# Kernel optimization log

Hardware: AMD Instinct MI355X
Metric: run time of the kernel (lower is better)

## Reference

```python
import jax, jax.numpy as jnp
import numpy as np

B, T, D, H = 2048, 200, 64, 64


def setup_inputs() -> dict:
    key = jax.random.key(0)
    ks = jax.random.split(key, 5)
    rnn_input = jax.random.normal(ks[0], (B, T, D), dtype=jnp.float32)
    sequence_length = jax.random.randint(ks[1], (B,), 0, T, dtype=jnp.int32)
    att_score = jax.random.uniform(ks[2], (B, T, 1), dtype=jnp.float32)
    # glorot-uniform-style init for kernels; TF VecAttGRUCell uses constant 1.0 gate bias
    s = np.float32(np.sqrt(6.0 / (D + H + 2 * H)))
    gate_kernel = jax.random.uniform(ks[3], (D + H, 2 * H), jnp.float32, -s, s)
    gate_bias = jnp.ones((2 * H,), jnp.float32)
    sc = np.float32(np.sqrt(6.0 / (D + H + H)))
    cand_kernel = jax.random.uniform(ks[4], (D + H, H), jnp.float32, -sc, sc)
    cand_bias = jnp.zeros((H,), jnp.float32)
    return dict(rnn_input=rnn_input, sequence_length=sequence_length,
                att_score=att_score, gate_kernel=gate_kernel, gate_bias=gate_bias,
                cand_kernel=cand_kernel, cand_bias=cand_bias)


def _augru(rnn_input, sequence_length, att_score, gate_kernel, gate_bias, cand_kernel, cand_bias):
    # rnn_input: [B,T,D], att_score: [B,T,1], sequence_length: [B]
    Bn, Tn, _ = rnn_input.shape
    Hn = cand_kernel.shape[1]
    x_t = jnp.swapaxes(rnn_input, 0, 1)   # [T,B,D]
    a_t = jnp.swapaxes(att_score, 0, 1)   # [T,B,1]
    t_idx = jnp.arange(Tn)
    h0 = jnp.zeros((Bn, Hn), rnn_input.dtype)

    def step(h, inp):
        x, a, t = inp
        gates = jax.nn.sigmoid(jnp.concatenate([x, h], axis=-1) @ gate_kernel + gate_bias)
        r, u = jnp.split(gates, 2, axis=-1)                       # [B,H] each
        c = jnp.tanh(jnp.concatenate([x, r * h], axis=-1) @ cand_kernel + cand_bias)
        u_hat = (1.0 - a) * u                                      # attention-modulated update gate
        new_h = u_hat * h + (1.0 - u_hat) * c
        valid = (t < sequence_length)[:, None]                     # dynamic_rnn semantics
        h_next = jnp.where(valid, new_h, h)                        # freeze state past seq len
        out = jnp.where(valid, new_h, jnp.zeros_like(new_h))       # zero outputs past seq len
        return h_next, out

    h_last, outs = jax.lax.scan(step, h0, (x_t, a_t, t_idx))
    return jnp.swapaxes(outs, 0, 1), h_last  # [B,T,H], [B,H]


def reference(rnn_input, sequence_length, att_score, gate_kernel, gate_bias, cand_kernel, cand_bias):
    outputs, _ = _augru(rnn_input, sequence_length, att_score,
                        gate_kernel, gate_bias, cand_kernel, cand_bias)
    return outputs  # return_sequence=True
```

## Files before the change

kernel.cpp:

```cpp
#include <hip/hip_runtime.h>

#define Tn 200
#define Dn 64
#define Hn 64
#define CC 16

typedef _Float16 half2v __attribute__((ext_vector_type(2)));
typedef _Float16 half8v __attribute__((ext_vector_type(8)));
typedef float    f32x4  __attribute__((ext_vector_type(4)));

__device__ __forceinline__ float fast_sigmoid(float v) {
    return __builtin_amdgcn_rcpf(1.0f + __expf(-v));
}
__device__ __forceinline__ float fast_tanh(float v) {
    return 1.0f - 2.0f * __builtin_amdgcn_rcpf(1.0f + __expf(2.0f * v));
}
__device__ __forceinline__ void wave_lds_fence() {
    asm volatile("s_waitcnt lgkmcnt(0)" ::: "memory");
}

__device__ __forceinline__ half8v cvt8(const float4 a, const float4 b) {
    return half8v{(_Float16)a.x, (_Float16)a.y, (_Float16)a.z, (_Float16)a.w,
                  (_Float16)b.x, (_Float16)b.y, (_Float16)b.z, (_Float16)b.w};
}

__global__ __launch_bounds__(256, 4)
void augru_proj_mfma(const float* __restrict__ x,
                     const int*   __restrict__ slen,
                     const float* __restrict__ gk,
                     const float* __restrict__ gb,
                     const float* __restrict__ ck,
                     const float* __restrict__ cb,
                     _Float16*    __restrict__ P,
                     int nrows, int nchunks)
{
    const int tid  = threadIdx.x;
    const int w    = tid >> 6;
    const int lane = tid & 63;
    const int lm   = lane & 15;
    const int kq   = lane >> 4;

    half8v bf[3][2];
    float  bias[3];
#pragma unroll
    for (int nt = 0; nt < 3; ++nt) {
        const int n = w * 48 + nt * 16 + lm;
#pragma unroll
        for (int kh = 0; kh < 2; ++kh) {
            const int kb = kh * 32 + kq * 8;
            half8v f;
#pragma unroll
            for (int e = 0; e < 8; ++e) {
                const int k = kb + e;
                const float v = (n < 128) ? gk[k * 128 + n]
                                          : ck[k * 64 + (n - 128)];
                f[e] = (_Float16)v;
            }
            bf[nt][kh] = f;
        }
        bias[nt] = (n < 128) ? gb[n] : cb[n - 128];
    }

    for (int chunk = blockIdx.x; chunk < nchunks; chunk += gridDim.x) {
        const int rb0 = chunk * 64;
#pragma unroll
        for (int sub = 0; sub < 4; ++sub) {
            const int rb = rb0 + sub * 16;

            const int rowv = rb + lm;
            const int bv   = rowv / Tn;
            const int tv   = rowv - bv * Tn;
            const bool v   = (rowv < nrows) && (tv < slen[bv]);
            if (__ballot(v) == 0ull) continue;

            const int rowA = min(rb + lm, nrows - 1);
            const float* xr = x + (size_t)rowA * Dn + kq * 8;
            const float4 q0 = *(const float4*)(xr);
            const float4 q1 = *(const float4*)(xr + 4);
            const float4 q2 = *(const float4*)(xr + 32);
            const float4 q3 = *(const float4*)(xr + 36);
            const half8v a0 = cvt8(q0, q1);
            const half8v a1 = cvt8(q2, q3);

            f32x4 acc[3];
#pragma unroll
            for (int nt = 0; nt < 3; ++nt) {
                f32x4 c = {bias[nt], bias[nt], bias[nt], bias[nt]};
                c = __builtin_amdgcn_mfma_f32_16x16x32_f16(a0, bf[nt][0], c, 0, 0, 0);
                c = __builtin_amdgcn_mfma_f32_16x16x32_f16(a1, bf[nt][1], c, 0, 0, 0);
                acc[nt] = c;
            }

#pragma unroll
            for (int r = 0; r < 4; ++r) {
                const int row = rb + kq * 4 + r;
                const int bb  = row / Tn;
                const int tt  = row - bb * Tn;
                if (row < nrows && tt < slen[bb]) {
                    _Float16* Pt = P + (size_t)row * 192 + w * 48 + lm;
                    Pt[0]  = (_Float16)acc[0][r];
                    Pt[16] = (_Float16)acc[1][r];
                    Pt[32] = (_Float16)acc[2][r];
                }
            }
        }
    }
}

__global__ __launch_bounds__(64, 2)
void augru_rec(const _Float16* __restrict__ P,
               const int*     __restrict__ slen,
               const float*   __restrict__ att,
               const float*   __restrict__ gk,
               const float*   __restrict__ ck,
               float*         __restrict__ out)
{
    const int b = blockIdx.x;
    const int j = threadIdx.x;

    __shared__ __align__(16) _Float16 s_h[Hn];
    __shared__ __align__(16) _Float16 s_rh[Hn];

    half2v wr[32], wu[32], wc[32];
#pragma unroll
    for (int m = 0; m < 32; ++m) {
        const int k = 64 + 2 * m;
        wr[m] = half2v{(_Float16)gk[(k + 0) * 128 + j],
                       (_Float16)gk[(k + 1) * 128 + j]};
        wu[m] = half2v{(_Float16)gk[(k + 0) * 128 + 64 + j],
                       (_Float16)gk[(k + 1) * 128 + 64 + j]};
        wc[m] = half2v{(_Float16)ck[(k + 0) * 64 + j],
                       (_Float16)ck[(k + 1) * 64 + j]};
    }

    const int len = slen[b];
    const _Float16* Prow = P   + (size_t)b * Tn * 192;
    const float*    arow = att + (size_t)b * Tn;
    float*          orow = out + (size_t)b * Tn * Hn;

    float h = 0.0f;

    _Float16 pr_n = (_Float16)0, pu_n = (_Float16)0, pc_n = (_Float16)0;
    float a_n = 0.0f;
    if (len > 0) {
        pr_n = Prow[j]; pu_n = Prow[64 + j]; pc_n = Prow[128 + j];
        a_n  = arow[0];
    }

    for (int t = 0; t < len; ++t) {
        const float pr = (float)pr_n;
        const float pu = (float)pu_n;
        const float pc = (float)pc_n;
        const float a  = a_n;
        const int tn = min(t + 1, len - 1);
        const _Float16* Pt = Prow + tn * 192;
        pr_n = Pt[j]; pu_n = Pt[64 + j]; pc_n = Pt[128 + j];
        a_n  = arow[tn];

        s_h[j] = (_Float16)h;
        wave_lds_fence();

        float r0 = pr, r1 = 0.f, u0 = pu, u1 = 0.f;
        const half8v* hv = (const half8v*)s_h;
#pragma unroll
        for (int m8 = 0; m8 < 8; ++m8) {
            const half8v v = hv[m8];
            const half2v p0 = __builtin_shufflevector(v, v, 0, 1);
            const half2v p1 = __builtin_shufflevector(v, v, 2, 3);
            const half2v p2 = __builtin_shufflevector(v, v, 4, 5);
            const half2v p3 = __builtin_shufflevector(v, v, 6, 7);
            const int m = m8 * 4;
            r0 = __builtin_amdgcn_fdot2(p0, wr[m + 0], r0, false);
            r1 = __builtin_amdgcn_fdot2(p1, wr[m + 1], r1, false);
            r0 = __builtin_amdgcn_fdot2(p2, wr[m + 2], r0, false);
            r1 = __builtin_amdgcn_fdot2(p3, wr[m + 3], r1, false);
            u0 = __builtin_amdgcn_fdot2(p0, wu[m + 0], u0, false);
            u1 = __builtin_amdgcn_fdot2(p1, wu[m + 1], u1, false);
            u0 = __builtin_amdgcn_fdot2(p2, wu[m + 2], u0, false);
            u1 = __builtin_amdgcn_fdot2(p3, wu[m + 3], u1, false);
        }
        const float rg = fast_sigmoid(r0 + r1);
        const float ug = fast_sigmoid(u0 + u1);

        s_rh[j] = (_Float16)(rg * h);
        wave_lds_fence();

        float c0 = pc, c1 = 0.f;
        const half8v* rv = (const half8v*)s_rh;
#pragma unroll
        for (int m8 = 0; m8 < 8; ++m8) {
            const half8v v = rv[m8];
            const half2v p0 = __builtin_shufflevector(v, v, 0, 1);
            const half2v p1 = __builtin_shufflevector(v, v, 2, 3);
            const half2v p2 = __builtin_shufflevector(v, v, 4, 5);
            const half2v p3 = __builtin_shufflevector(v, v, 6, 7);
            const int m = m8 * 4;
            c0 = __builtin_amdgcn_fdot2(p0, wc[m + 0], c0, false);
            c1 = __builtin_amdgcn_fdot2(p1, wc[m + 1], c1, false);
            c0 = __builtin_amdgcn_fdot2(p2, wc[m + 2], c0, false);
            c1 = __builtin_amdgcn_fdot2(p3, wc[m + 3], c1, false);
        }
        const float cg = fast_tanh(c0 + c1);

        const float uh = (1.0f - a) * ug;
        h = uh * h + (1.0f - uh) * cg;
        orow[t * Hn + j] = h;
        wave_lds_fence();
    }

    float4 z;
    z.x = z.y = z.z = z.w = 0.0f;
    float* tail = orow + len * Hn;
    const int total = (Tn - len) * Hn;
    for (int i = j * 4; i < total; i += 64 * 4) {
        *(float4*)(tail + i) = z;
    }
}

__global__ __launch_bounds__(128, 2)
void augru_fused_fb(const float* __restrict__ x, const int* __restrict__ slen,
                    const float* __restrict__ att, const float* __restrict__ gk,
                    const float* __restrict__ gb, const float* __restrict__ ck,
                    const float* __restrict__ cb, float* __restrict__ out)
{
    const int b    = blockIdx.x;
    const int tid  = threadIdx.x;
    const int wave = tid >> 6;
    const int j    = tid & 63;

    __shared__ float s_P[2][CC][3][Hn];
    __shared__ __align__(16) _Float16 s_h[Hn];
    __shared__ __align__(16) _Float16 s_rh[Hn];

    const int len     = slen[b];
    const int nchunks = (len + CC - 1) / CC;
    const float* xrow = x   + (size_t)b * Tn * Dn;
    const float* arow = att + (size_t)b * Tn;
    float*       orow = out + (size_t)b * Tn * Hn;

    if (wave == 0) {
        half2v wr[32], wu[32], wc[32];
#pragma unroll
        for (int m = 0; m < 32; ++m) {
            const int k = 2 * m;
            wr[m] = half2v{(_Float16)gk[(k + 0) * 128 + j], (_Float16)gk[(k + 1) * 128 + j]};
            wu[m] = half2v{(_Float16)gk[(k + 0) * 128 + 64 + j], (_Float16)gk[(k + 1) * 128 + 64 + j]};
            wc[m] = half2v{(_Float16)ck[(k + 0) * 64 + j], (_Float16)ck[(k + 1) * 64 + j]};
        }
        const float br = gb[j], bu = gb[64 + j], bc = cb[j];
        for (int c = 0; c < nchunks; ++c) {
            const int t0 = c * CC, tend = min(len, t0 + CC);
            for (int t = t0; t < tend; ++t) {
                const float4* xv = (const float4*)(xrow + t * Dn);
                float r0 = br, r1 = 0.f, u0 = bu, u1 = 0.f, c0 = bc, c1 = 0.f;
#pragma unroll
                for (int kk = 0; kk < 16; ++kk) {
                    const float4 q = xv[kk];
                    const half2v p0 = half2v{(_Float16)q.x, (_Float16)q.y};
                    const half2v p1 = half2v{(_Float16)q.z, (_Float16)q.w};
                    const int m = 2 * kk;
                    r0 = __builtin_amdgcn_fdot2(p0, wr[m], r0, false);
                    r1 = __builtin_amdgcn_fdot2(p1, wr[m + 1], r1, false);
                    u0 = __builtin_amdgcn_fdot2(p0, wu[m], u0, false);
                    u1 = __builtin_amdgcn_fdot2(p1, wu[m + 1], u1, false);
                    c0 = __builtin_amdgcn_fdot2(p0, wc[m], c0, false);
                    c1 = __builtin_amdgcn_fdot2(p1, wc[m + 1], c1, false);
                }
                const int lt = t - t0;
                s_P[c & 1][lt][0][j] = r0 + r1;
                s_P[c & 1][lt][1][j] = u0 + u1;
                s_P[c & 1][lt][2][j] = c0 + c1;
            }
            __syncthreads();
        }
    } else {
        half2v wr[32], wu[32], wc[32];
#pragma unroll
        for (int m = 0; m < 32; ++m) {
            const int k = 64 + 2 * m;
            wr[m] = half2v{(_Float16)gk[(k + 0) * 128 + j], (_Float16)gk[(k + 1) * 128 + j]};
            wu[m] = half2v{(_Float16)gk[(k + 0) * 128 + 64 + j], (_Float16)gk[(k + 1) * 128 + 64 + j]};
            wc[m] = half2v{(_Float16)ck[(k + 0) * 64 + j], (_Float16)ck[(k + 1) * 64 + j]};
        }
        float h = 0.0f;
        for (int c = 0; c < nchunks; ++c) {
            __syncthreads();
            const int t0 = c * CC, tend = min(len, t0 + CC);
            for (int t = t0; t < tend; ++t) {
                const int lt = t - t0;
                const float pr = s_P[c & 1][lt][0][j];
                const float pu = s_P[c & 1][lt][1][j];
                const float pc = s_P[c & 1][lt][2][j];
                const float a  = arow[t];
                s_h[j] = (_Float16)h;
                wave_lds_fence();
                float r0 = pr, r1 = 0.f, u0 = pu, u1 = 0.f;
                const half8v* hv = (const half8v*)s_h;
#pragma unroll
                for (int m8 = 0; m8 < 8; ++m8) {
                    const half8v v = hv[m8];
                    const half2v p0 = __builtin_shufflevector(v, v, 0, 1);
                    const half2v p1 = __builtin_shufflevector(v, v, 2, 3);
                    const half2v p2 = __builtin_shufflevector(v, v, 4, 5);
                    const half2v p3 = __builtin_shufflevector(v, v, 6, 7);
                    const int m = m8 * 4;
                    r0 = __builtin_amdgcn_fdot2(p0, wr[m + 0], r0, false);
                    r1 = __builtin_amdgcn_fdot2(p1, wr[m + 1], r1, false);
                    r0 = __builtin_amdgcn_fdot2(p2, wr[m + 2], r0, false);
                    r1 = __builtin_amdgcn_fdot2(p3, wr[m + 3], r1, false);
                    u0 = __builtin_amdgcn_fdot2(p0, wu[m + 0], u0, false);
                    u1 = __builtin_amdgcn_fdot2(p1, wu[m + 1], u1, false);
                    u0 = __builtin_amdgcn_fdot2(p2, wu[m + 2], u0, false);
                    u1 = __builtin_amdgcn_fdot2(p3, wu[m + 3], u1, false);
                }
                const float rg = fast_sigmoid(r0 + r1);
                const float ug = fast_sigmoid(u0 + u1);
                s_rh[j] = (_Float16)(rg * h);
                wave_lds_fence();
                float c0 = pc, c1 = 0.f;
                const half8v* rv = (const half8v*)s_rh;
#pragma unroll
                for (int m8 = 0; m8 < 8; ++m8) {
                    const half8v v = rv[m8];
                    const half2v p0 = __builtin_shufflevector(v, v, 0, 1);
                    const half2v p1 = __builtin_shufflevector(v, v, 2, 3);
                    const half2v p2 = __builtin_shufflevector(v, v, 4, 5);
                    const half2v p3 = __builtin_shufflevector(v, v, 6, 7);
                    const int m = m8 * 4;
                    c0 = __builtin_amdgcn_fdot2(p0, wc[m + 0], c0, false);
                    c1 = __builtin_amdgcn_fdot2(p1, wc[m + 1], c1, false);
                    c0 = __builtin_amdgcn_fdot2(p2, wc[m + 2], c0, false);
                    c1 = __builtin_amdgcn_fdot2(p3, wc[m + 3], c1, false);
                }
                const float cg = fast_tanh(c0 + c1);
                const float uh = (1.0f - a) * ug;
                h = uh * h + (1.0f - uh) * cg;
                orow[t * Hn + j] = h;
                wave_lds_fence();
            }
        }
    }
    float4 z; z.x = z.y = z.z = z.w = 0.0f;
    float* tail = orow + len * Hn;
    const int total = (Tn - len) * Hn;
    for (int i = tid * 4; i < total; i += 128 * 4) *(float4*)(tail + i) = z;
}

extern "C" void kernel_launch(void* const* d_in, const int* in_sizes, int n_in,
                              void* d_out, int out_size, void* d_ws, size_t ws_size,
                              hipStream_t stream) {
    const float* x    = (const float*)d_in[0];
    const int*   slen = (const int*)  d_in[1];
    const float* att  = (const float*)d_in[2];
    const float* gk   = (const float*)d_in[3];
    const float* gb   = (const float*)d_in[4];
    const float* ck   = (const float*)d_in[5];
    const float* cb   = (const float*)d_in[6];
    float* out = (float*)d_out;

    const int B = in_sizes[1];
    const size_t needP = (size_t)B * Tn * 192 * sizeof(_Float16);

    if (ws_size >= needP) {
        _Float16* P = (_Float16*)d_ws;
        const int nrows   = B * Tn;
        const int nchunks = (nrows + 63) / 64;
        const int grid    = nchunks < 1024 ? nchunks : 1024;
        augru_proj_mfma<<<grid, 256, 0, stream>>>(x, slen, gk, gb, ck, cb, P,
                                                  nrows, nchunks);
        augru_rec<<<B, 64, 0, stream>>>(P, slen, att, gk, ck, out);
    } else {
        augru_fused_fb<<<B, 128, 0, stream>>>(x, slen, att, gk, gb, ck, cb, out);
    }
}
```

Before: 370.3 us.

## Ping-pong LDS buffers and reorder recurrent step to shorten per-step critical path

The recurrent kernel's step loop is unrolled by two. It alternates between two sets of LDS buffers, which lets the trailing fence at the end of each step be dropped. The reset-gate dot product now runs first, so r*h can be written to LDS while the update-gate dot product is still computing, and each dot product uses four accumulators instead of two to shorten dependency chains. Prefetch distance for the projections and attention values goes from one step ahead to two. The cost is more registers and reliance on the alternating buffers to prevent write-after-read hazards within the single wave.

```diff
diff --git a/kernel.cpp b/kernel.cpp
--- a/kernel.cpp
+++ b/kernel.cpp
@@ -23,6 +23,16 @@
     return half8v{(_Float16)a.x, (_Float16)a.y, (_Float16)a.z, (_Float16)a.w,
                   (_Float16)b.x, (_Float16)b.y, (_Float16)b.z, (_Float16)b.w};
 }
+
+#define DOT8(v, W, mb, a0, a1, a2, a3)                                  \
+    {   const half2v q0 = __builtin_shufflevector(v, v, 0, 1);          \
+        const half2v q1 = __builtin_shufflevector(v, v, 2, 3);          \
+        const half2v q2 = __builtin_shufflevector(v, v, 4, 5);          \
+        const half2v q3 = __builtin_shufflevector(v, v, 6, 7);          \
+        a0 = __builtin_amdgcn_fdot2(q0, W[(mb) + 0], a0, false);        \
+        a1 = __builtin_amdgcn_fdot2(q1, W[(mb) + 1], a1, false);        \
+        a2 = __builtin_amdgcn_fdot2(q2, W[(mb) + 2], a2, false);        \
+        a3 = __builtin_amdgcn_fdot2(q3, W[(mb) + 3], a3, false);        }
 
 __global__ __launch_bounds__(256, 4)
 void augru_proj_mfma(const float* __restrict__ x,
@@ -107,6 +117,80 @@
     }
 }
 
+__device__ __forceinline__ float augru_step(
+    float h, int t, int len, int j,
+    const _Float16* __restrict__ Prow, const float* __restrict__ arow,
+    float* __restrict__ orow,
+    _Float16& pr_s, _Float16& pu_s, _Float16& pc_s, float& a_s,
+    const half2v* __restrict__ wr, const half2v* __restrict__ wu,
+    const half2v* __restrict__ wc,
+    _Float16* __restrict__ sh, _Float16* __restrict__ srh)
+{
+    const float pr = (float)pr_s;
+    const float pu = (float)pu_s;
+    const float pc = (float)pc_s;
+    const float a  = a_s;
+
+    const int tn = min(t + 2, len - 1);
+    const _Float16* Pt = Prow + (size_t)tn * 192;
+    pr_s = Pt[j]; pu_s = Pt[64 + j]; pc_s = Pt[128 + j];
+    a_s  = arow[tn];
+
+    sh[j] = (_Float16)h;
+    wave_lds_fence();
+
+    const half8v* hv = (const half8v*)sh;
+    const half8v v0 = hv[0], v1 = hv[1], v2 = hv[2], v3 = hv[3];
+    const half8v v4 = hv[4], v5 = hv[5], v6 = hv[6], v7 = hv[7];
+
+    float r0 = pr, r1 = 0.f, r2 = 0.f, r3 = 0.f;
+    DOT8(v0, wr,  0, r0, r1, r2, r3);
+    DOT8(v1, wr,  4, r0, r1, r2, r3);
+    DOT8(v2, wr,  8, r0, r1, r2, r3);
+    DOT8(v3, wr, 12, r0, r1, r2, r3);
+    DOT8(v4, wr, 16, r0, r1, r2, r3);
+    DOT8(v5, wr, 20, r0, r1, r2, r3);
+    DOT8(v6, wr, 24, r0, r1, r2, r3);
+    DOT8(v7, wr, 28, r0, r1, r2, r3);
+    const float rg = fast_sigmoid((r0 + r1) + (r2 + r3));
+
+    srh[j] = (_Float16)(rg * h);
+
+    float u0 = pu, u1 = 0.f, u2 = 0.f, u3 = 0.f;
+    DOT8(v0, wu,  0, u0, u1, u2, u3);
+    DOT8(v1, wu,  4, u0, u1, u2, u3);
+    DOT8(v2, wu,  8, u0, u1, u2, u3);
+    DOT8(v3, wu, 12, u0, u1, u2, u3);
+    DOT8(v4, wu, 16, u0, u1, u2, u3);
+    DOT8(v5, wu, 20, u0, u1, u2, u3);
+    DOT8(v6, wu, 24, u0, u1, u2, u3);
+    DOT8(v7, wu, 28, u0, u1, u2, u3);
+    const float ug = fast_sigmoid((u0 + u1) + (u2 + u3));
+
+    wave_lds_fence();
+
+    const half8v* rv = (const half8v*)srh;
+    float c0 = pc, c1 = 0.f, c2 = 0.f, c3 = 0.f;
+    {
+        const half8v w0 = rv[0], w1 = rv[1], w2 = rv[2], w3 = rv[3];
+        const half8v w4 = rv[4], w5 = rv[5], w6 = rv[6], w7 = rv[7];
+        DOT8(w0, wc,  0, c0, c1, c2, c3);
+        DOT8(w1, wc,  4, c0, c1, c2, c3);
+        DOT8(w2, wc,  8, c0, c1, c2, c3);
+        DOT8(w3, wc, 12, c0, c1, c2, c3);
+        DOT8(w4, wc, 16, c0, c1, c2, c3);
+        DOT8(w5, wc, 20, c0, c1, c2, c3);
+        DOT8(w6, wc, 24, c0, c1, c2, c3);
+        DOT8(w7, wc, 28, c0, c1, c2, c3);
+    }
+    const float cg = fast_tanh((c0 + c1) + (c2 + c3));
+
+    const float uh = (1.0f - a) * ug;
+    h = uh * h + (1.0f - uh) * cg;
+    orow[(size_t)t * Hn + j] = h;
+    return h;
+}
+
 __global__ __launch_bounds__(64, 2)
 void augru_rec(const _Float16* __restrict__ P,
                const int*     __restrict__ slen,
@@ -118,8 +202,10 @@
     const int b = blockIdx.x;
     const int j = threadIdx.x;
 
-    __shared__ __align__(16) _Float16 s_h[Hn];
-    __shared__ __align__(16) _Float16 s_rh[Hn];
+    __shared__ __align__(16) _Float16 s_h0[Hn];
+    __shared__ __align__(16) _Float16 s_rh0[Hn];
+    __shared__ __align__(16) _Float16 s_h1[Hn];
+    __shared__ __align__(16) _Float16 s_rh1[Hn];
 
     half2v wr[32], wu[32], wc[32];
 #pragma unroll
@@ -140,77 +226,28 @@
 
     float h = 0.0f;
 
-    _Float16 pr_n = (_Float16)0, pu_n = (_Float16)0, pc_n = (_Float16)0;
-    float a_n = 0.0f;
     if (len > 0) {
-        pr_n = Prow[j]; pu_n = Prow[64 + j]; pc_n = Prow[128 + j];
-        a_n  = arow[0];
-    }
-
-    for (int t = 0; t < len; ++t) {
-        const float pr = (float)pr_n;
-        const float pu = (float)pu_n;
-        const float pc = (float)pc_n;
-        const float a  = a_n;
-        const int tn = min(t + 1, len - 1);
-        const _Float16* Pt = Prow + tn * 192;
-        pr_n = Pt[j]; pu_n = Pt[64 + j]; pc_n = Pt[128 + j];
-        a_n  = arow[tn];
-
-        s_h[j] = (_Float16)h;
-        wave_lds_fence();
-
-        float r0 = pr, r1 = 0.f, u0 = pu, u1 = 0.f;
-        const half8v* hv = (const half8v*)s_h;
-#pragma unroll
-        for (int m8 = 0; m8 < 8; ++m8) {
-            const half8v v = hv[m8];
-            const half2v p0 = __builtin_shufflevector(v, v, 0, 1);
-            const half2v p1 = __builtin_shufflevector(v, v, 2, 3);
-            const half2v p2 = __builtin_shufflevector(v, v, 4, 5);
-            const half2v p3 = __builtin_shufflevector(v, v, 6, 7);
-            const int m = m8 * 4;
-            r0 = __builtin_amdgcn_fdot2(p0, wr[m + 0], r0, false);
-            r1 = __builtin_amdgcn_fdot2(p1, wr[m + 1], r1, false);
-            r0 = __builtin_amdgcn_fdot2(p2, wr[m + 2], r0, false);
-            r1 = __builtin_amdgcn_fdot2(p3, wr[m + 3], r1, false);
-            u0 = __builtin_amdgcn_fdot2(p0, wu[m + 0], u0, false);
-            u1 = __builtin_amdgcn_fdot2(p1, wu[m + 1], u1, false);
-            u0 = __builtin_amdgcn_fdot2(p2, wu[m + 2], u0, false);
-            u1 = __builtin_amdgcn_fdot2(p3, wu[m + 3], u1, false);
-        }
-        const float rg = fast_sigmoid(r0 + r1);
-        const float ug = fast_sigmoid(u0 + u1);
-
-        s_rh[j] = (_Float16)(rg * h);
-        wave_lds_fence();
-
-        float c0 = pc, c1 = 0.f;
-        const half8v* rv = (const half8v*)s_rh;
-#pragma unroll
-        for (int m8 = 0; m8 < 8; ++m8) {
-            const half8v v = rv[m8];
-            const half2v p0 = __builtin_shufflevector(v, v, 0, 1);
-            const half2v p1 = __builtin_shufflevector(v, v, 2, 3);
-            const half2v p2 = __builtin_shufflevector(v, v, 4, 5);
-            const half2v p3 = __builtin_shufflevector(v, v, 6, 7);
-            const int m = m8 * 4;
-            c0 = __builtin_amdgcn_fdot2(p0, wc[m + 0], c0, false);
-            c1 = __builtin_amdgcn_fdot2(p1, wc[m + 1], c1, false);
-            c0 = __builtin_amdgcn_fdot2(p2, wc[m + 2], c0, false);
-            c1 = __builtin_amdgcn_fdot2(p3, wc[m + 3], c1, false);
-        }
-        const float cg = fast_tanh(c0 + c1);
-
-        const float uh = (1.0f - a) * ug;
-        h = uh * h + (1.0f - uh) * cg;
-        orow[t * Hn + j] = h;
-        wave_lds_fence();
+        _Float16 prA = Prow[j], puA = Prow[64 + j], pcA = Prow[128 + j];
+        float    aA  = arow[0];
+        const int t1 = min(1, len - 1);
+        const _Float16* P1 = Prow + (size_t)t1 * 192;
+        _Float16 prB = P1[j], puB = P1[64 + j], pcB = P1[128 + j];
+        float    aB  = arow[t1];
+
+        int t = 0;
+        while (true) {
+            h = augru_step(h, t, len, j, Prow, arow, orow,
+                           prA, puA, pcA, aA, wr, wu, wc, s_h0, s_rh0);
+            ++t; if (t >= len) break;
+            h = augru_step(h, t, len, j, Prow, arow, orow,
+                           prB, puB, pcB, aB, wr, wu, wc, s_h1, s_rh1);
+            ++t; if (t >= len) break;
+        }
     }
 
     float4 z;
     z.x = z.y = z.z = z.w = 0.0f;
-    float* tail = orow + len * Hn;
+    float* tail = orow + (size_t)len * Hn;
     const int total = (Tn - len) * Hn;
     for (int i = j * 4; i < total; i += 64 * 4) {
         *(float4*)(tail + i) = z;
```

Result: no change. 373.9 us (+1.0%).
